# Optimization experiments

Hardware: AMD Instinct MI355X
Metric: run time of the kernel (lower is better)

## Reference

```python
import jax, jax.numpy as jnp
import numpy as np

B, T, I, H, O = 1024, 128, 128, 1024, 64


def setup_inputs() -> dict:
    key = jax.random.key(0)
    ks = jax.random.split(key, 7)
    s_i = 1.0 / np.sqrt(H)
    return {
        "x": jax.random.normal(ks[0], (B, T * I), dtype=jnp.float32),
        "w_ih": jax.random.uniform(ks[1], (4 * H, I), minval=-s_i, maxval=s_i, dtype=jnp.float32),
        "w_hh": jax.random.uniform(ks[2], (4 * H, H), minval=-s_i, maxval=s_i, dtype=jnp.float32),
        "b_ih": jax.random.uniform(ks[3], (4 * H,), minval=-s_i, maxval=s_i, dtype=jnp.float32),
        "b_hh": jax.random.uniform(ks[4], (4 * H,), minval=-s_i, maxval=s_i, dtype=jnp.float32),
        "w_fc": jax.random.uniform(ks[5], (O, H), minval=-s_i, maxval=s_i, dtype=jnp.float32),
        "b_fc": jax.random.uniform(ks[6], (O,), minval=-s_i, maxval=s_i, dtype=jnp.float32),
    }


def reference(x, w_ih, w_hh, b_ih, b_hh, w_fc, b_fc):
    b = x.shape[0]
    i_dim = w_ih.shape[1]
    h_dim = w_hh.shape[1]
    t = x.shape[1] // i_dim
    # chunk(dim=1) into t contiguous slices == reshape [b, t, i]
    xs = x.reshape(b, t, i_dim)
    # precompute input-to-gate projection for all timesteps in one GEMM
    xg = jnp.einsum("bti,gi->tbg", xs, w_ih) + (b_ih + b_hh)  # [t, b, 4h]

    def step(carry, xg_t):
        h, c = carry
        gates = xg_t + h @ w_hh.T  # [b, 4h]
        ig, fg, gg, og = jnp.split(gates, 4, axis=-1)  # PyTorch LSTMCell gate order
        c_new = jax.nn.sigmoid(fg) * c + jax.nn.sigmoid(ig) * jnp.tanh(gg)
        h_new = jax.nn.sigmoid(og) * jnp.tanh(c_new)
        return (h_new, c_new), None

    h0 = jnp.zeros((b, h_dim), dtype=x.dtype)
    c0 = jnp.zeros((b, h_dim), dtype=x.dtype)
    (h_t, _), _ = jax.lax.scan(step, (h0, c0), xg)
    return h_t @ w_fc.T + b_fc
```

## Files before the change

### kernel.cpp

```cpp
#include <hip/hip_runtime.h>


#define B_DIM 1024
#define H_DIM 1024
#define I_DIM 128
#define T_DIM 128
#define XROW  (T_DIM * I_DIM)
#define KDIM  (I_DIM + H_DIM)
#define GDIM  (4 * H_DIM)
#define O_DIM 64

typedef float f32x4 __attribute__((ext_vector_type(4)));
typedef short bf16x8 __attribute__((ext_vector_type(8)));
typedef unsigned short u16x8 __attribute__((ext_vector_type(8)));

__device__ __forceinline__ unsigned short f2bf(float f) {
    union { float f; unsigned int u; } v; v.f = f;
    unsigned int r = v.u + 0x7fffu + ((v.u >> 16) & 1u);
    return (unsigned short)(r >> 16);
}
__device__ __forceinline__ float bf2f(unsigned short b) {
    union { unsigned int u; float f; } v; v.u = ((unsigned int)b) << 16;
    return v.f;
}
__device__ __forceinline__ float sigm(float x) { return 1.f / (1.f + __expf(-x)); }
__device__ __forceinline__ float tanh_fast(float x) { return 2.f / (1.f + __expf(-2.f * x)) - 1.f; }

__global__ void conv_x(const float* __restrict__ x, unsigned short* __restrict__ xb) {
    size_t i = ((size_t)blockIdx.x * 256 + threadIdx.x) * 8;
    float4 v0 = *(const float4*)(x + i);
    float4 v1 = *(const float4*)(x + i + 4);
    u16x8 o;
    o[0] = f2bf(v0.x); o[1] = f2bf(v0.y); o[2] = f2bf(v0.z); o[3] = f2bf(v0.w);
    o[4] = f2bf(v1.x); o[5] = f2bf(v1.y); o[6] = f2bf(v1.z); o[7] = f2bf(v1.w);
    *(u16x8*)(xb + i) = o;
}

__global__ void build_w(const float* __restrict__ w_ih, const float* __restrict__ w_hh,
                        const float* __restrict__ b_ih, const float* __restrict__ b_hh,
                        unsigned short* __restrict__ W, float* __restrict__ bias) {
    int r = blockIdx.x;
    int nb = r >> 7, q = r & 127;
    int wh = q >> 6, w = q & 63;
    int gate = w >> 4, jl = w & 15;
    int orig = gate * 1024 + nb * 32 + wh * 16 + jl;
    for (int k = threadIdx.x; k < KDIM; k += 256) {
        float v = (k < I_DIM) ? w_ih[(size_t)orig * I_DIM + k]
                              : w_hh[(size_t)orig * H_DIM + (k - I_DIM)];
        W[(size_t)r * KDIM + k] = f2bf(v);
    }
    if (threadIdx.x == 0) bias[r] = b_ih[orig] + b_hh[orig];
}

__global__ void trans_wfc(const float* __restrict__ w_fc, float* __restrict__ wT) {
    int o = blockIdx.x;
    for (int k = threadIdx.x; k < H_DIM; k += 256)
        wT[(size_t)k * O_DIM + o] = w_fc[(size_t)o * H_DIM + k];
}

__global__ void zero_hc(unsigned short* __restrict__ h0, float* __restrict__ c) {
    int idx = blockIdx.x * 256 + threadIdx.x;
    h0[idx] = 0;
    c[idx] = 0.f;
}

#define READ_TILE(OFF) do {                                                       \
    asm volatile("ds_read_b128 %0, %1 offset:" OFF : "=v"(fa0) : "v"(aA0));       \
    asm volatile("ds_read_b128 %0, %1 offset:" OFF : "=v"(fa1) : "v"(aA1));       \
    asm volatile("ds_read_b128 %0, %1 offset:" OFF : "=v"(fb0) : "v"(aB0));       \
    asm volatile("ds_read_b128 %0, %1 offset:" OFF : "=v"(fb1) : "v"(aB1));       \
    asm volatile("ds_read_b128 %0, %1 offset:" OFF : "=v"(fb2) : "v"(aB2));       \
    asm volatile("ds_read_b128 %0, %1 offset:" OFF : "=v"(fb3) : "v"(aB3));       \
    asm volatile("ds_read_b128 %0, %1 offset:" OFF : "=v"(ga0) : "v"(aA0x));      \
    asm volatile("ds_read_b128 %0, %1 offset:" OFF : "=v"(ga1) : "v"(aA1x));      \
    asm volatile("ds_read_b128 %0, %1 offset:" OFF : "=v"(gb0) : "v"(aB0x));      \
    asm volatile("ds_read_b128 %0, %1 offset:" OFF : "=v"(gb1) : "v"(aB1x));      \
    asm volatile("ds_read_b128 %0, %1 offset:" OFF : "=v"(gb2) : "v"(aB2x));      \
    asm volatile("ds_read_b128 %0, %1 offset:" OFF : "=v"(gb3) : "v"(aB3x));      \
    asm volatile("s_waitcnt lgkmcnt(0)" ::: "memory");                            \
    __builtin_amdgcn_sched_barrier(0);                                            \
} while (0)

#define MFMA_(a, b, c) c = __builtin_amdgcn_mfma_f32_16x16x32_bf16(a, b, c, 0, 0, 0)
#define MM_TILE() do {                                                            \
    MFMA_(fa0, fb0, acc[0][0]); MFMA_(fa0, fb1, acc[0][1]);                       \
    MFMA_(fa0, fb2, acc[0][2]); MFMA_(fa0, fb3, acc[0][3]);                       \
    MFMA_(fa1, fb0, acc[1][0]); MFMA_(fa1, fb1, acc[1][1]);                       \
    MFMA_(fa1, fb2, acc[1][2]); MFMA_(fa1, fb3, acc[1][3]);                       \
    MFMA_(ga0, gb0, acc[0][0]); MFMA_(ga0, gb1, acc[0][1]);                       \
    MFMA_(ga0, gb2, acc[0][2]); MFMA_(ga0, gb3, acc[0][3]);                       \
    MFMA_(ga1, gb0, acc[1][0]); MFMA_(ga1, gb1, acc[1][1]);                       \
    MFMA_(ga1, gb2, acc[1][2]); MFMA_(ga1, gb3, acc[1][3]);                       \
} while (0)

__global__ __launch_bounds__(512, 2)
void lstm_step(const unsigned short* __restrict__ xb,
               const unsigned short* __restrict__ W,
               const float* __restrict__ bias,
               const unsigned short* __restrict__ h_in,
               unsigned short* __restrict__ h_out,
               float* __restrict__ c_st,
               int t) {
    __shared__ __align__(16) unsigned short lds[4 * 8192];
    const int tid  = threadIdx.x;
    const int wv   = tid >> 6, lane = tid & 63;
    const int wm   = wv >> 1, wn = wv & 1;
    const int quad = lane >> 4, l16 = lane & 15;
    const int l7   = l16 & 7;
    const int bid = blockIdx.x;
    const int xcd = bid & 7;
    const int sl  = bid >> 3;
    const int nb  = xcd * 4 + (sl & 3);
    const int mb  = sl >> 2;

    const int j  = nb * 32 + wn * 16 + l16;
    const int bb = nb * 128 + wn * 64 + l16;
    const float bi  = bias[bb +  0];
    const float bf_ = bias[bb + 16];
    const float bg  = bias[bb + 32];
    const float bo  = bias[bb + 48];
    float cold[2][4];
#pragma unroll
    for (int mi = 0; mi < 2; mi++)
#pragma unroll
        for (int r = 0; r < 4; r++) {
            const int brow = mb * 128 + wm * 32 + mi * 16 + quad * 4 + r;
            cold[mi][r] = c_st[(size_t)brow * H_DIM + j];
        }

    f32x4 acc[2][4];
#pragma unroll
    for (int i = 0; i < 2; i++)
#pragma unroll
        for (int jj = 0; jj < 4; jj++) acc[i][jj] = f32x4{0.f, 0.f, 0.f, 0.f};

    const int arow = lane >> 3;
    const int ag   = lane & 7;
    const int colperm = ((ag ^ arow) << 3);

    auto stage = [&](int bsel, int ks) {
        const int kt = ks * 64;
        unsigned short* As_ = lds + bsel * 16384;
        unsigned short* Bs_ = As_ + 8192;
#pragma unroll
        for (int c4 = 0; c4 < 2; ++c4) {
            const int row0 = wv * 16 + c4 * 8;
            const int row  = row0 + arow;
            const unsigned short* srcA =
                (kt < I_DIM)
                    ? xb   + (size_t)(mb * 128 + row) * XROW + t * I_DIM + kt + colperm
                    : h_in + (size_t)(mb * 128 + row) * H_DIM + (kt - I_DIM) + colperm;
            __builtin_amdgcn_global_load_lds(
                (const __attribute__((address_space(1))) void*)srcA,
                (__attribute__((address_space(3))) void*)(&As_[row0 * 64]), 16, 0, 0);
        }
#pragma unroll
        for (int c4 = 0; c4 < 2; ++c4) {
            const int row0 = wv * 16 + c4 * 8;
            const int row  = row0 + arow;
            const unsigned short* srcB =
                W + (size_t)(nb * 128 + row) * KDIM + kt + colperm;
            __builtin_amdgcn_global_load_lds(
                (const __attribute__((address_space(1))) void*)srcB,
                (__attribute__((address_space(3))) void*)(&Bs_[row0 * 64]), 16, 0, 0);
        }
    };

    const unsigned lbase = (unsigned)(unsigned long long)
        (__attribute__((address_space(3))) void*)lds;
    const unsigned cp  = (unsigned)((quad ^ l7) << 4);
    const unsigned aA0 = lbase + (unsigned)((wm * 32 + l16) * 128) + cp;
    const unsigned aA1 = aA0 + 2048;
    const unsigned aB0 = lbase + 16384u + (unsigned)((wn * 64 + l16) * 128) + cp;
    const unsigned aB1 = aB0 + 2048;
    const unsigned aB2 = aB0 + 4096;
    const unsigned aB3 = aB0 + 6144;
    const unsigned aA0x = aA0 ^ 64u, aA1x = aA1 ^ 64u;
    const unsigned aB0x = aB0 ^ 64u, aB1x = aB1 ^ 64u;
    const unsigned aB2x = aB2 ^ 64u, aB3x = aB3 ^ 64u;
    bf16x8 fa0, fa1, fb0, fb1, fb2, fb3, ga0, ga1, gb0, gb1, gb2, gb3;

    stage(0, 0);
    stage(1, 1);
#pragma unroll 1
    for (int p = 0; p < 8; ++p) {
        asm volatile("s_waitcnt vmcnt(4)" ::: "memory");
        __builtin_amdgcn_s_barrier();
        READ_TILE("0");
        __builtin_amdgcn_s_barrier();
        stage(0, 2 * p + 2);
        MM_TILE();

        asm volatile("s_waitcnt vmcnt(4)" ::: "memory");
        __builtin_amdgcn_s_barrier();
        READ_TILE("32768");
        __builtin_amdgcn_s_barrier();
        stage(1, 2 * p + 3);
        MM_TILE();
    }
    asm volatile("s_waitcnt vmcnt(4)" ::: "memory");
    __builtin_amdgcn_s_barrier();
    READ_TILE("0");
    MM_TILE();
    asm volatile("s_waitcnt vmcnt(0)" ::: "memory");
    __builtin_amdgcn_s_barrier();
    READ_TILE("32768");
    MM_TILE();

#pragma unroll
    for (int mi = 0; mi < 2; mi++) {
#pragma unroll
        for (int r = 0; r < 4; r++) {
            const int brow = mb * 128 + wm * 32 + mi * 16 + quad * 4 + r;
            const float gi = acc[mi][0][r] + bi;
            const float gf = acc[mi][1][r] + bf_;
            const float gg = acc[mi][2][r] + bg;
            const float go = acc[mi][3][r] + bo;
            const size_t idx = (size_t)brow * H_DIM + j;
            const float cn = sigm(gf) * cold[mi][r] + sigm(gi) * tanh_fast(gg);
            c_st[idx] = cn;
            h_out[idx] = f2bf(sigm(go) * tanh_fast(cn));
        }
    }
}

__global__ void proj(const unsigned short* __restrict__ h,
                     const float* __restrict__ wT,
                     const float* __restrict__ b_fc,
                     float* __restrict__ out) {
    __shared__ float hs[4][H_DIM];
    const int tid = threadIdx.x, wv = tid >> 6, o = tid & 63;
    const int b = blockIdx.x * 4 + wv;
    const unsigned short* hrow = h + (size_t)b * H_DIM;
#pragma unroll
    for (int i = 0; i < 2; ++i) {
        const int k0 = i * 512 + o * 8;
        u16x8 v = *(const u16x8*)(hrow + k0);
        float4 f0 = {bf2f((unsigned short)v[0]), bf2f((unsigned short)v[1]),
                     bf2f((unsigned short)v[2]), bf2f((unsigned short)v[3])};
        float4 f1 = {bf2f((unsigned short)v[4]), bf2f((unsigned short)v[5]),
                     bf2f((unsigned short)v[6]), bf2f((unsigned short)v[7])};
        *(float4*)&hs[wv][k0]     = f0;
        *(float4*)&hs[wv][k0 + 4] = f1;
    }
    float s0 = 0.f, s1 = 0.f, s2 = 0.f, s3 = 0.f;
#pragma unroll 4
    for (int k4 = 0; k4 < H_DIM / 4; ++k4) {
        float4 hv = *(const float4*)&hs[wv][k4 * 4];
        const float* wp = wT + (size_t)k4 * 4 * O_DIM + o;
        s0 += hv.x * wp[0 * O_DIM];
        s1 += hv.y * wp[1 * O_DIM];
        s2 += hv.z * wp[2 * O_DIM];
        s3 += hv.w * wp[3 * O_DIM];
    }
    out[(size_t)b * O_DIM + o] = s0 + s1 + s2 + s3 + b_fc[o];
}

extern "C" void kernel_launch(void* const* d_in, const int* in_sizes, int n_in,
                              void* d_out, int out_size, void* d_ws, size_t ws_size,
                              hipStream_t stream) {
    const float* x    = (const float*)d_in[0];
    const float* w_ih = (const float*)d_in[1];
    const float* w_hh = (const float*)d_in[2];
    const float* b_ih = (const float*)d_in[3];
    const float* b_hh = (const float*)d_in[4];
    const float* w_fc = (const float*)d_in[5];
    const float* b_fc = (const float*)d_in[6];
    float* out = (float*)d_out;

    char* ws = (char*)d_ws;
    size_t off = 0;
    unsigned short* xb = (unsigned short*)(ws + off); off += (size_t)B_DIM * XROW * 2;
    unsigned short* W  = (unsigned short*)(ws + off); off += (size_t)GDIM * KDIM * 2;
    float* bias        = (float*)(ws + off);          off += (size_t)GDIM * 4;
    unsigned short* h0 = (unsigned short*)(ws + off); off += (size_t)B_DIM * H_DIM * 2;
    unsigned short* h1 = (unsigned short*)(ws + off); off += (size_t)B_DIM * H_DIM * 2;
    float* c           = (float*)(ws + off);          off += (size_t)B_DIM * H_DIM * 4;
    float* wT          = (float*)(ws + off);          off += (size_t)H_DIM * O_DIM * 4;

    conv_x<<<8192, 256, 0, stream>>>(x, xb);
    build_w<<<GDIM, 256, 0, stream>>>(w_ih, w_hh, b_ih, b_hh, W, bias);
    trans_wfc<<<O_DIM, 256, 0, stream>>>(w_fc, wT);
    zero_hc<<<4096, 256, 0, stream>>>(h0, c);

    for (int t = 0; t < T_DIM; ++t) {
        const unsigned short* hin = (t & 1) ? h1 : h0;
        unsigned short* hout      = (t & 1) ? h0 : h1;
        lstm_step<<<256, 512, 0, stream>>>(xb, W, bias, hin, hout, c, t);
    }
    proj<<<256, 256, 0, stream>>>(h0, wT, b_fc, out);
}
```

Before: 1.976 ms.

## Load A operands directly to registers, keep only B in LDS

The A operand (x slice and hidden state) is no longer staged through LDS. It is loaded straight into registers with global_load_dwordx4 in MFMA fragment layout and double-buffered across k-steps, so only the weight tile goes through LDS, which halves the shared-memory footprint. The aim is to cut LDS traffic and ds_read work per tile and raise occupancy headroom. In exchange it adds VGPR pressure for the prefetched A registers, uses uncoalesced per-lane global loads, and relies on fragile hand-tuned vmcnt counts.

```diff
diff --git a/kernel.cpp b/kernel.cpp
--- a/kernel.cpp
+++ b/kernel.cpp
@@ -64,15 +64,11 @@
     c[idx] = 0.f;
 }
 
-#define READ_TILE(OFF) do {                                                       \
-    asm volatile("ds_read_b128 %0, %1 offset:" OFF : "=v"(fa0) : "v"(aA0));       \
-    asm volatile("ds_read_b128 %0, %1 offset:" OFF : "=v"(fa1) : "v"(aA1));       \
+#define READ_B(OFF) do {                                                          \
     asm volatile("ds_read_b128 %0, %1 offset:" OFF : "=v"(fb0) : "v"(aB0));       \
     asm volatile("ds_read_b128 %0, %1 offset:" OFF : "=v"(fb1) : "v"(aB1));       \
     asm volatile("ds_read_b128 %0, %1 offset:" OFF : "=v"(fb2) : "v"(aB2));       \
     asm volatile("ds_read_b128 %0, %1 offset:" OFF : "=v"(fb3) : "v"(aB3));       \
-    asm volatile("ds_read_b128 %0, %1 offset:" OFF : "=v"(ga0) : "v"(aA0x));      \
-    asm volatile("ds_read_b128 %0, %1 offset:" OFF : "=v"(ga1) : "v"(aA1x));      \
     asm volatile("ds_read_b128 %0, %1 offset:" OFF : "=v"(gb0) : "v"(aB0x));      \
     asm volatile("ds_read_b128 %0, %1 offset:" OFF : "=v"(gb1) : "v"(aB1x));      \
     asm volatile("ds_read_b128 %0, %1 offset:" OFF : "=v"(gb2) : "v"(aB2x));      \
@@ -81,16 +77,27 @@
     __builtin_amdgcn_sched_barrier(0);                                            \
 } while (0)
 
+#define ISSUE_A(T0, T1, T2, T3, V0, V1, BASE, O0, O1) do {                         \
+    asm volatile("global_load_dwordx4 %0, %1, %2 offset:" O0                       \
+                 : "=v"(T0) : "v"(V0), "s"(BASE));                                 \
+    asm volatile("global_load_dwordx4 %0, %1, %2 offset:" O0                       \
+                 : "=v"(T1) : "v"(V1), "s"(BASE));                                 \
+    asm volatile("global_load_dwordx4 %0, %1, %2 offset:" O1                       \
+                 : "=v"(T2) : "v"(V0), "s"(BASE));                                 \
+    asm volatile("global_load_dwordx4 %0, %1, %2 offset:" O1                       \
+                 : "=v"(T3) : "v"(V1), "s"(BASE));                                 \
+} while (0)
+
 #define MFMA_(a, b, c) c = __builtin_amdgcn_mfma_f32_16x16x32_bf16(a, b, c, 0, 0, 0)
-#define MM_TILE() do {                                                            \
-    MFMA_(fa0, fb0, acc[0][0]); MFMA_(fa0, fb1, acc[0][1]);                       \
-    MFMA_(fa0, fb2, acc[0][2]); MFMA_(fa0, fb3, acc[0][3]);                       \
-    MFMA_(fa1, fb0, acc[1][0]); MFMA_(fa1, fb1, acc[1][1]);                       \
-    MFMA_(fa1, fb2, acc[1][2]); MFMA_(fa1, fb3, acc[1][3]);                       \
-    MFMA_(ga0, gb0, acc[0][0]); MFMA_(ga0, gb1, acc[0][1]);                       \
-    MFMA_(ga0, gb2, acc[0][2]); MFMA_(ga0, gb3, acc[0][3]);                       \
-    MFMA_(ga1, gb0, acc[1][0]); MFMA_(ga1, gb1, acc[1][1]);                       \
-    MFMA_(ga1, gb2, acc[1][2]); MFMA_(ga1, gb3, acc[1][3]);                       \
+#define MM_TILE(A0, A1, A2, A3) do {                                              \
+    MFMA_(A0, fb0, acc[0][0]); MFMA_(A0, fb1, acc[0][1]);                         \
+    MFMA_(A0, fb2, acc[0][2]); MFMA_(A0, fb3, acc[0][3]);                         \
+    MFMA_(A1, fb0, acc[1][0]); MFMA_(A1, fb1, acc[1][1]);                         \
+    MFMA_(A1, fb2, acc[1][2]); MFMA_(A1, fb3, acc[1][3]);                         \
+    MFMA_(A2, gb0, acc[0][0]); MFMA_(A2, gb1, acc[0][1]);                         \
+    MFMA_(A2, gb2, acc[0][2]); MFMA_(A2, gb3, acc[0][3]);                         \
+    MFMA_(A3, gb0, acc[1][0]); MFMA_(A3, gb1, acc[1][1]);                         \
+    MFMA_(A3, gb2, acc[1][2]); MFMA_(A3, gb3, acc[1][3]);                         \
 } while (0)
 
 __global__ __launch_bounds__(512, 2)
@@ -101,7 +108,7 @@
                unsigned short* __restrict__ h_out,
                float* __restrict__ c_st,
                int t) {
-    __shared__ __align__(16) unsigned short lds[4 * 8192];
+    __shared__ __align__(16) unsigned short lds[2 * 8192];
     const int tid  = threadIdx.x;
     const int wv   = tid >> 6, lane = tid & 63;
     const int wm   = wv >> 1, wn = wv & 1;
@@ -138,22 +145,9 @@
     const int ag   = lane & 7;
     const int colperm = ((ag ^ arow) << 3);
 
-    auto stage = [&](int bsel, int ks) {
+    auto stageB = [&](int bsel, int ks) {
         const int kt = ks * 64;
-        unsigned short* As_ = lds + bsel * 16384;
-        unsigned short* Bs_ = As_ + 8192;
-#pragma unroll
-        for (int c4 = 0; c4 < 2; ++c4) {
-            const int row0 = wv * 16 + c4 * 8;
-            const int row  = row0 + arow;
-            const unsigned short* srcA =
-                (kt < I_DIM)
-                    ? xb   + (size_t)(mb * 128 + row) * XROW + t * I_DIM + kt + colperm
-                    : h_in + (size_t)(mb * 128 + row) * H_DIM + (kt - I_DIM) + colperm;
-            __builtin_amdgcn_global_load_lds(
-                (const __attribute__((address_space(1))) void*)srcA,
-                (__attribute__((address_space(3))) void*)(&As_[row0 * 64]), 16, 0, 0);
-        }
+        unsigned short* Bs_ = lds + bsel * 8192;
 #pragma unroll
         for (int c4 = 0; c4 < 2; ++c4) {
             const int row0 = wv * 16 + c4 * 8;
@@ -169,43 +163,59 @@
     const unsigned lbase = (unsigned)(unsigned long long)
         (__attribute__((address_space(3))) void*)lds;
     const unsigned cp  = (unsigned)((quad ^ l7) << 4);
-    const unsigned aA0 = lbase + (unsigned)((wm * 32 + l16) * 128) + cp;
-    const unsigned aA1 = aA0 + 2048;
-    const unsigned aB0 = lbase + 16384u + (unsigned)((wn * 64 + l16) * 128) + cp;
+    const unsigned aB0 = lbase + (unsigned)((wn * 64 + l16) * 128) + cp;
     const unsigned aB1 = aB0 + 2048;
     const unsigned aB2 = aB0 + 4096;
     const unsigned aB3 = aB0 + 6144;
-    const unsigned aA0x = aA0 ^ 64u, aA1x = aA1 ^ 64u;
     const unsigned aB0x = aB0 ^ 64u, aB1x = aB1 ^ 64u;
     const unsigned aB2x = aB2 ^ 64u, aB3x = aB3 ^ 64u;
-    bf16x8 fa0, fa1, fb0, fb1, fb2, fb3, ga0, ga1, gb0, gb1, gb2, gb3;
-
-    stage(0, 0);
-    stage(1, 1);
+    bf16x8 fb0, fb1, fb2, fb3, gb0, gb1, gb2, gb3;
+
+    const int rowA0 = mb * 128 + wm * 32 + l16;
+    const int rowA1 = rowA0 + 16;
+    unsigned voffX0 = (unsigned)((rowA0 * XROW + t * I_DIM + quad * 8) * 2);
+    unsigned voffX1 = (unsigned)((rowA1 * XROW + t * I_DIM + quad * 8) * 2);
+    unsigned voffH0 = (unsigned)((rowA0 * H_DIM + quad * 8) * 2);
+    unsigned voffH1 = (unsigned)((rowA1 * H_DIM + quad * 8) * 2);
+    bf16x8 pa0, pa1, pa2, pa3;
+    bf16x8 qa0, qa1, qa2, qa3;
+
+    stageB(0, 0);
+    ISSUE_A(pa0, pa1, pa2, pa3, voffX0, voffX1, xb, "0", "64");
+    ISSUE_A(qa0, qa1, qa2, qa3, voffX0, voffX1, xb, "128", "192");
+    stageB(1, 1);
+
+    asm volatile("s_waitcnt vmcnt(6)" ::: "memory");
+    __builtin_amdgcn_s_barrier();
+    READ_B("0");
+    __builtin_amdgcn_s_barrier();
+    stageB(0, 2);
+    MM_TILE(pa0, pa1, pa2, pa3);
+
 #pragma unroll 1
     for (int p = 0; p < 8; ++p) {
-        asm volatile("s_waitcnt vmcnt(4)" ::: "memory");
+        asm volatile("s_waitcnt vmcnt(2)" ::: "memory");
         __builtin_amdgcn_s_barrier();
-        READ_TILE("0");
+        READ_B("16384");
         __builtin_amdgcn_s_barrier();
-        stage(0, 2 * p + 2);
-        MM_TILE();
-
-        asm volatile("s_waitcnt vmcnt(4)" ::: "memory");
+        ISSUE_A(pa0, pa1, pa2, pa3, voffH0, voffH1, h_in, "0", "64");
+        voffH0 += 128; voffH1 += 128;
+        stageB(1, 2 * p + 3);
+        MM_TILE(qa0, qa1, qa2, qa3);
+
+        asm volatile("s_waitcnt vmcnt(2)" ::: "memory");
         __builtin_amdgcn_s_barrier();
-        READ_TILE("32768");
+        READ_B("0");
         __builtin_amdgcn_s_barrier();
-        stage(1, 2 * p + 3);
-        MM_TILE();
-    }
-    asm volatile("s_waitcnt vmcnt(4)" ::: "memory");
-    __builtin_amdgcn_s_barrier();
-    READ_TILE("0");
-    MM_TILE();
+        ISSUE_A(qa0, qa1, qa2, qa3, voffH0, voffH1, h_in, "0", "64");
+        voffH0 += 128; voffH1 += 128;
+        if (p < 7) stageB(0, 2 * p + 4);
+        MM_TILE(pa0, pa1, pa2, pa3);
+    }
     asm volatile("s_waitcnt vmcnt(0)" ::: "memory");
     __builtin_amdgcn_s_barrier();
-    READ_TILE("32768");
-    MM_TILE();
+    READ_B("16384");
+    MM_TILE(qa0, qa1, qa2, qa3);
 
 #pragma unroll
     for (int mi = 0; mi < 2; mi++) {
```

Result: slower. 3.948 ms (+99.8%).

## Halve threads per LSTM step block, give each wave a 64x64 tile

Applied to the files above, without the earlier changes.

Each block now runs 4 waves of 256 threads instead of 8. Each wave computes a 64x64 output tile with 16 accumulators instead of 32x64, which gives more register-level reuse of A and B fragments per LDS read. Staging issues 4 loads per operand per wave, and the prologue, main loop and epilogue are reorganised to match. The final tile splits its LDS wait so the first half of the MFMAs can start before all reads land. The cost is lower occupancy and fewer waves available to hide latency, plus higher register pressure.

```diff
diff --git a/kernel.cpp b/kernel.cpp
--- a/kernel.cpp
+++ b/kernel.cpp
@@ -67,33 +67,56 @@
 #define READ_TILE(OFF) do {                                                       \
     asm volatile("ds_read_b128 %0, %1 offset:" OFF : "=v"(fa0) : "v"(aA0));       \
     asm volatile("ds_read_b128 %0, %1 offset:" OFF : "=v"(fa1) : "v"(aA1));       \
+    asm volatile("ds_read_b128 %0, %1 offset:" OFF : "=v"(fa2) : "v"(aA2));       \
+    asm volatile("ds_read_b128 %0, %1 offset:" OFF : "=v"(fa3) : "v"(aA3));       \
     asm volatile("ds_read_b128 %0, %1 offset:" OFF : "=v"(fb0) : "v"(aB0));       \
     asm volatile("ds_read_b128 %0, %1 offset:" OFF : "=v"(fb1) : "v"(aB1));       \
     asm volatile("ds_read_b128 %0, %1 offset:" OFF : "=v"(fb2) : "v"(aB2));       \
     asm volatile("ds_read_b128 %0, %1 offset:" OFF : "=v"(fb3) : "v"(aB3));       \
-    asm volatile("ds_read_b128 %0, %1 offset:" OFF : "=v"(ga0) : "v"(aA0x));      \
-    asm volatile("ds_read_b128 %0, %1 offset:" OFF : "=v"(ga1) : "v"(aA1x));      \
-    asm volatile("ds_read_b128 %0, %1 offset:" OFF : "=v"(gb0) : "v"(aB0x));      \
-    asm volatile("ds_read_b128 %0, %1 offset:" OFF : "=v"(gb1) : "v"(aB1x));      \
-    asm volatile("ds_read_b128 %0, %1 offset:" OFF : "=v"(gb2) : "v"(aB2x));      \
-    asm volatile("ds_read_b128 %0, %1 offset:" OFF : "=v"(gb3) : "v"(aB3x));      \
-    asm volatile("s_waitcnt lgkmcnt(0)" ::: "memory");                            \
-    __builtin_amdgcn_sched_barrier(0);                                            \
+    asm volatile("ds_read_b128 %0, %1 offset:" OFF : "=v"(ga0) : "v"(aA0 ^ 64u)); \
+    asm volatile("ds_read_b128 %0, %1 offset:" OFF : "=v"(ga1) : "v"(aA1 ^ 64u)); \
+    asm volatile("ds_read_b128 %0, %1 offset:" OFF : "=v"(ga2) : "v"(aA2 ^ 64u)); \
+    asm volatile("ds_read_b128 %0, %1 offset:" OFF : "=v"(ga3) : "v"(aA3 ^ 64u)); \
+    asm volatile("ds_read_b128 %0, %1 offset:" OFF : "=v"(gb0) : "v"(aB0 ^ 64u)); \
+    asm volatile("ds_read_b128 %0, %1 offset:" OFF : "=v"(gb1) : "v"(aB1 ^ 64u)); \
+    asm volatile("ds_read_b128 %0, %1 offset:" OFF : "=v"(gb2) : "v"(aB2 ^ 64u)); \
+    asm volatile("ds_read_b128 %0, %1 offset:" OFF : "=v"(gb3) : "v"(aB3 ^ 64u)); \
 } while (0)
 
 #define MFMA_(a, b, c) c = __builtin_amdgcn_mfma_f32_16x16x32_bf16(a, b, c, 0, 0, 0)
-#define MM_TILE() do {                                                            \
+
+#define MM_HALF1() do {                                                           \
     MFMA_(fa0, fb0, acc[0][0]); MFMA_(fa0, fb1, acc[0][1]);                       \
     MFMA_(fa0, fb2, acc[0][2]); MFMA_(fa0, fb3, acc[0][3]);                       \
     MFMA_(fa1, fb0, acc[1][0]); MFMA_(fa1, fb1, acc[1][1]);                       \
     MFMA_(fa1, fb2, acc[1][2]); MFMA_(fa1, fb3, acc[1][3]);                       \
+    MFMA_(fa2, fb0, acc[2][0]); MFMA_(fa2, fb1, acc[2][1]);                       \
+    MFMA_(fa2, fb2, acc[2][2]); MFMA_(fa2, fb3, acc[2][3]);                       \
+    MFMA_(fa3, fb0, acc[3][0]); MFMA_(fa3, fb1, acc[3][1]);                       \
+    MFMA_(fa3, fb2, acc[3][2]); MFMA_(fa3, fb3, acc[3][3]);                       \
+} while (0)
+#define MM_HALF2() do {                                                           \
     MFMA_(ga0, gb0, acc[0][0]); MFMA_(ga0, gb1, acc[0][1]);                       \
     MFMA_(ga0, gb2, acc[0][2]); MFMA_(ga0, gb3, acc[0][3]);                       \
     MFMA_(ga1, gb0, acc[1][0]); MFMA_(ga1, gb1, acc[1][1]);                       \
     MFMA_(ga1, gb2, acc[1][2]); MFMA_(ga1, gb3, acc[1][3]);                       \
+    MFMA_(ga2, gb0, acc[2][0]); MFMA_(ga2, gb1, acc[2][1]);                       \
+    MFMA_(ga2, gb2, acc[2][2]); MFMA_(ga2, gb3, acc[2][3]);                       \
+    MFMA_(ga3, gb0, acc[3][0]); MFMA_(ga3, gb1, acc[3][1]);                       \
+    MFMA_(ga3, gb2, acc[3][2]); MFMA_(ga3, gb3, acc[3][3]);                       \
 } while (0)
 
-__global__ __launch_bounds__(512, 2)
+#define DO_TILE(OFF) do {                                                         \
+    READ_TILE(OFF);                                                               \
+    asm volatile("s_waitcnt lgkmcnt(8)" ::: "memory");                            \
+    __builtin_amdgcn_sched_barrier(0);                                            \
+    MM_HALF1();                                                                   \
+    asm volatile("s_waitcnt lgkmcnt(0)" ::: "memory");                            \
+    __builtin_amdgcn_sched_barrier(0);                                            \
+    MM_HALF2();                                                                   \
+} while (0)
+
+__global__ __launch_bounds__(256, 1)
 void lstm_step(const unsigned short* __restrict__ xb,
                const unsigned short* __restrict__ W,
                const float* __restrict__ bias,
@@ -101,7 +124,7 @@
                unsigned short* __restrict__ h_out,
                float* __restrict__ c_st,
                int t) {
-    __shared__ __align__(16) unsigned short lds[4 * 8192];
+    __shared__ __align__(16) unsigned short lds[2 * 16384];
     const int tid  = threadIdx.x;
     const int wv   = tid >> 6, lane = tid & 63;
     const int wm   = wv >> 1, wn = wv & 1;
@@ -119,18 +142,18 @@
     const float bf_ = bias[bb + 16];
     const float bg  = bias[bb + 32];
     const float bo  = bias[bb + 48];
-    float cold[2][4];
-#pragma unroll
-    for (int mi = 0; mi < 2; mi++)
+    float cold[4][4];
+#pragma unroll
+    for (int mi = 0; mi < 4; mi++)
 #pragma unroll
         for (int r = 0; r < 4; r++) {
-            const int brow = mb * 128 + wm * 32 + mi * 16 + quad * 4 + r;
+            const int brow = mb * 128 + wm * 64 + mi * 16 + quad * 4 + r;
             cold[mi][r] = c_st[(size_t)brow * H_DIM + j];
         }
 
-    f32x4 acc[2][4];
-#pragma unroll
-    for (int i = 0; i < 2; i++)
+    f32x4 acc[4][4];
+#pragma unroll
+    for (int i = 0; i < 4; i++)
 #pragma unroll
         for (int jj = 0; jj < 4; jj++) acc[i][jj] = f32x4{0.f, 0.f, 0.f, 0.f};
 
@@ -143,8 +166,8 @@
         unsigned short* As_ = lds + bsel * 16384;
         unsigned short* Bs_ = As_ + 8192;
 #pragma unroll
-        for (int c4 = 0; c4 < 2; ++c4) {
-            const int row0 = wv * 16 + c4 * 8;
+        for (int c4 = 0; c4 < 4; ++c4) {
+            const int row0 = wv * 32 + c4 * 8;
             const int row  = row0 + arow;
             const unsigned short* srcA =
                 (kt < I_DIM)
@@ -155,8 +178,8 @@
                 (__attribute__((address_space(3))) void*)(&As_[row0 * 64]), 16, 0, 0);
         }
 #pragma unroll
-        for (int c4 = 0; c4 < 2; ++c4) {
-            const int row0 = wv * 16 + c4 * 8;
+        for (int c4 = 0; c4 < 4; ++c4) {
+            const int row0 = wv * 32 + c4 * 8;
             const int row  = row0 + arow;
             const unsigned short* srcB =
                 W + (size_t)(nb * 128 + row) * KDIM + kt + colperm;
@@ -169,49 +192,60 @@
     const unsigned lbase = (unsigned)(unsigned long long)
         (__attribute__((address_space(3))) void*)lds;
     const unsigned cp  = (unsigned)((quad ^ l7) << 4);
-    const unsigned aA0 = lbase + (unsigned)((wm * 32 + l16) * 128) + cp;
+    const unsigned aA0 = lbase + (unsigned)((wm * 64 + l16) * 128) + cp;
     const unsigned aA1 = aA0 + 2048;
+    const unsigned aA2 = aA0 + 4096;
+    const unsigned aA3 = aA0 + 6144;
     const unsigned aB0 = lbase + 16384u + (unsigned)((wn * 64 + l16) * 128) + cp;
     const unsigned aB1 = aB0 + 2048;
     const unsigned aB2 = aB0 + 4096;
     const unsigned aB3 = aB0 + 6144;
-    const unsigned aA0x = aA0 ^ 64u, aA1x = aA1 ^ 64u;
-    const unsigned aB0x = aB0 ^ 64u, aB1x = aB1 ^ 64u;
-    const unsigned aB2x = aB2 ^ 64u, aB3x = aB3 ^ 64u;
-    bf16x8 fa0, fa1, fb0, fb1, fb2, fb3, ga0, ga1, gb0, gb1, gb2, gb3;
+    bf16x8 fa0, fa1, fa2, fa3, fb0, fb1, fb2, fb3;
+    bf16x8 ga0, ga1, ga2, ga3, gb0, gb1, gb2, gb3;
 
     stage(0, 0);
     stage(1, 1);
+    asm volatile("s_waitcnt vmcnt(8)" ::: "memory");
+    __builtin_amdgcn_s_barrier();
+    READ_TILE("0");
+    asm volatile("s_waitcnt lgkmcnt(0)" ::: "memory");
+    __builtin_amdgcn_sched_barrier(0);
+    __builtin_amdgcn_s_barrier();
+    stage(0, 2);
+    MM_HALF1();
+    MM_HALF2();
+
 #pragma unroll 1
     for (int p = 0; p < 8; ++p) {
-        asm volatile("s_waitcnt vmcnt(4)" ::: "memory");
+        asm volatile("s_waitcnt vmcnt(8)" ::: "memory");
+        __builtin_amdgcn_s_barrier();
+        READ_TILE("32768");
+        asm volatile("s_waitcnt lgkmcnt(0)" ::: "memory");
+        __builtin_amdgcn_sched_barrier(0);
+        __builtin_amdgcn_s_barrier();
+        stage(1, 2 * p + 3);
+        MM_HALF1();
+        MM_HALF2();
+
+        asm volatile("s_waitcnt vmcnt(8)" ::: "memory");
         __builtin_amdgcn_s_barrier();
         READ_TILE("0");
+        asm volatile("s_waitcnt lgkmcnt(0)" ::: "memory");
+        __builtin_amdgcn_sched_barrier(0);
         __builtin_amdgcn_s_barrier();
-        stage(0, 2 * p + 2);
-        MM_TILE();
-
-        asm volatile("s_waitcnt vmcnt(4)" ::: "memory");
-        __builtin_amdgcn_s_barrier();
-        READ_TILE("32768");
-        __builtin_amdgcn_s_barrier();
-        stage(1, 2 * p + 3);
-        MM_TILE();
-    }
-    asm volatile("s_waitcnt vmcnt(4)" ::: "memory");
-    __builtin_amdgcn_s_barrier();
-    READ_TILE("0");
-    MM_TILE();
+        if (p < 7) stage(0, 2 * p + 4);
+        MM_HALF1();
+        MM_HALF2();
+    }
     asm volatile("s_waitcnt vmcnt(0)" ::: "memory");
     __builtin_amdgcn_s_barrier();
-    READ_TILE("32768");
-    MM_TILE();
-
-#pragma unroll
-    for (int mi = 0; mi < 2; mi++) {
+    DO_TILE("32768");
+
+#pragma unroll
+    for (int mi = 0; mi < 4; mi++) {
 #pragma unroll
         for (int r = 0; r < 4; r++) {
-            const int brow = mb * 128 + wm * 32 + mi * 16 + quad * 4 + r;
+            const int brow = mb * 128 + wm * 64 + mi * 16 + quad * 4 + r;
             const float gi = acc[mi][0][r] + bi;
             const float gf = acc[mi][1][r] + bf_;
             const float gg = acc[mi][2][r] + bg;
@@ -286,7 +320,7 @@
     for (int t = 0; t < T_DIM; ++t) {
         const unsigned short* hin = (t & 1) ? h1 : h0;
         unsigned short* hout      = (t & 1) ? h0 : h1;
-        lstm_step<<<256, 512, 0, stream>>>(xb, W, bias, hin, hout, c, t);
+        lstm_step<<<256, 256, 0, stream>>>(xb, W, bias, hin, hout, c, t);
     }
     proj<<<256, 256, 0, stream>>>(h0, wT, b_fc, out);
 }
```

Measured after the change: 2.104 ms. 6.5% more time.

## Deepen LSTM step GEMM pipeline to a four-stage LDS ring buffer

Applied to the files above, without the earlier changes.

Shared memory grows from two to four staging slots. The K-loop now prefetches three tiles ahead, and the barrier between reading a tile and refilling that slot is removed, so each k-tile pays one barrier instead of two. The goal is to hide more global-to-LDS latency in each latency-bound timestep GEMM. In exchange, LDS use doubles to 128 KB per block, which can limit how many blocks fit on a CU, and the vmcnt bookkeeping is hand-tuned and fragile.

```diff
diff --git a/kernel.cpp b/kernel.cpp
--- a/kernel.cpp
+++ b/kernel.cpp
@@ -64,19 +64,19 @@
     c[idx] = 0.f;
 }
 
-#define READ_TILE(OFF) do {                                                       \
-    asm volatile("ds_read_b128 %0, %1 offset:" OFF : "=v"(fa0) : "v"(aA0));       \
-    asm volatile("ds_read_b128 %0, %1 offset:" OFF : "=v"(fa1) : "v"(aA1));       \
-    asm volatile("ds_read_b128 %0, %1 offset:" OFF : "=v"(fb0) : "v"(aB0));       \
-    asm volatile("ds_read_b128 %0, %1 offset:" OFF : "=v"(fb1) : "v"(aB1));       \
-    asm volatile("ds_read_b128 %0, %1 offset:" OFF : "=v"(fb2) : "v"(aB2));       \
-    asm volatile("ds_read_b128 %0, %1 offset:" OFF : "=v"(fb3) : "v"(aB3));       \
-    asm volatile("ds_read_b128 %0, %1 offset:" OFF : "=v"(ga0) : "v"(aA0x));      \
-    asm volatile("ds_read_b128 %0, %1 offset:" OFF : "=v"(ga1) : "v"(aA1x));      \
-    asm volatile("ds_read_b128 %0, %1 offset:" OFF : "=v"(gb0) : "v"(aB0x));      \
-    asm volatile("ds_read_b128 %0, %1 offset:" OFF : "=v"(gb1) : "v"(aB1x));      \
-    asm volatile("ds_read_b128 %0, %1 offset:" OFF : "=v"(gb2) : "v"(aB2x));      \
-    asm volatile("ds_read_b128 %0, %1 offset:" OFF : "=v"(gb3) : "v"(aB3x));      \
+#define READ_TILE(A0, A1, B0, B1, B2, B3, OFF) do {                               \
+    asm volatile("ds_read_b128 %0, %1 offset:" OFF : "=v"(fa0) : "v"(A0));        \
+    asm volatile("ds_read_b128 %0, %1 offset:" OFF : "=v"(fa1) : "v"(A1));        \
+    asm volatile("ds_read_b128 %0, %1 offset:" OFF : "=v"(fb0) : "v"(B0));        \
+    asm volatile("ds_read_b128 %0, %1 offset:" OFF : "=v"(fb1) : "v"(B1));        \
+    asm volatile("ds_read_b128 %0, %1 offset:" OFF : "=v"(fb2) : "v"(B2));        \
+    asm volatile("ds_read_b128 %0, %1 offset:" OFF : "=v"(fb3) : "v"(B3));        \
+    asm volatile("ds_read_b128 %0, %1 offset:" OFF : "=v"(ga0) : "v"((A0) ^ 64u));\
+    asm volatile("ds_read_b128 %0, %1 offset:" OFF : "=v"(ga1) : "v"((A1) ^ 64u));\
+    asm volatile("ds_read_b128 %0, %1 offset:" OFF : "=v"(gb0) : "v"((B0) ^ 64u));\
+    asm volatile("ds_read_b128 %0, %1 offset:" OFF : "=v"(gb1) : "v"((B1) ^ 64u));\
+    asm volatile("ds_read_b128 %0, %1 offset:" OFF : "=v"(gb2) : "v"((B2) ^ 64u));\
+    asm volatile("ds_read_b128 %0, %1 offset:" OFF : "=v"(gb3) : "v"((B3) ^ 64u));\
     asm volatile("s_waitcnt lgkmcnt(0)" ::: "memory");                            \
     __builtin_amdgcn_sched_barrier(0);                                            \
 } while (0)
@@ -93,6 +93,11 @@
     MFMA_(ga1, gb2, acc[1][2]); MFMA_(ga1, gb3, acc[1][3]);                       \
 } while (0)
 
+#define WAITV(N) do {                                                             \
+    asm volatile("s_waitcnt vmcnt(" N ")" ::: "memory");                          \
+    __builtin_amdgcn_s_barrier();                                                 \
+} while (0)
+
 __global__ __launch_bounds__(512, 2)
 void lstm_step(const unsigned short* __restrict__ xb,
                const unsigned short* __restrict__ W,
@@ -101,7 +106,7 @@
                unsigned short* __restrict__ h_out,
                float* __restrict__ c_st,
                int t) {
-    __shared__ __align__(16) unsigned short lds[4 * 8192];
+    __shared__ __align__(16) unsigned short lds[8 * 8192];
     const int tid  = threadIdx.x;
     const int wv   = tid >> 6, lane = tid & 63;
     const int wm   = wv >> 1, wn = wv & 1;
@@ -175,36 +180,37 @@
     const unsigned aB1 = aB0 + 2048;
     const unsigned aB2 = aB0 + 4096;
     const unsigned aB3 = aB0 + 6144;
-    const unsigned aA0x = aA0 ^ 64u, aA1x = aA1 ^ 64u;
-    const unsigned aB0x = aB0 ^ 64u, aB1x = aB1 ^ 64u;
-    const unsigned aB2x = aB2 ^ 64u, aB3x = aB3 ^ 64u;
+    const unsigned cA0 = aA0 + 65536u, cA1 = aA1 + 65536u;
+    const unsigned cB0 = aB0 + 65536u, cB1 = aB1 + 65536u;
+    const unsigned cB2 = aB2 + 65536u, cB3 = aB3 + 65536u;
     bf16x8 fa0, fa1, fb0, fb1, fb2, fb3, ga0, ga1, gb0, gb1, gb2, gb3;
 
     stage(0, 0);
     stage(1, 1);
+    stage(2, 2);
+
 #pragma unroll 1
-    for (int p = 0; p < 8; ++p) {
-        asm volatile("s_waitcnt vmcnt(4)" ::: "memory");
-        __builtin_amdgcn_s_barrier();
-        READ_TILE("0");
-        __builtin_amdgcn_s_barrier();
-        stage(0, 2 * p + 2);
-        MM_TILE();
-
-        asm volatile("s_waitcnt vmcnt(4)" ::: "memory");
-        __builtin_amdgcn_s_barrier();
-        READ_TILE("32768");
-        __builtin_amdgcn_s_barrier();
-        stage(1, 2 * p + 3);
-        MM_TILE();
-    }
-    asm volatile("s_waitcnt vmcnt(4)" ::: "memory");
-    __builtin_amdgcn_s_barrier();
-    READ_TILE("0");
+    for (int q = 0; q < 3; ++q) {
+        WAITV("8"); READ_TILE(aA0, aA1, aB0, aB1, aB2, aB3, "0");
+        stage(3, 4 * q + 3); MM_TILE();
+        WAITV("8"); READ_TILE(aA0, aA1, aB0, aB1, aB2, aB3, "32768");
+        stage(0, 4 * q + 4); MM_TILE();
+        WAITV("8"); READ_TILE(cA0, cA1, cB0, cB1, cB2, cB3, "0");
+        stage(1, 4 * q + 5); MM_TILE();
+        WAITV("8"); READ_TILE(cA0, cA1, cB0, cB1, cB2, cB3, "32768");
+        stage(2, 4 * q + 6); MM_TILE();
+    }
+    WAITV("8"); READ_TILE(aA0, aA1, aB0, aB1, aB2, aB3, "0");
+    stage(3, 15); MM_TILE();
+    WAITV("8"); READ_TILE(aA0, aA1, aB0, aB1, aB2, aB3, "32768");
+    stage(0, 16); MM_TILE();
+    WAITV("8"); READ_TILE(cA0, cA1, cB0, cB1, cB2, cB3, "0");
+    stage(1, 17); MM_TILE();
+    WAITV("8"); READ_TILE(cA0, cA1, cB0, cB1, cB2, cB3, "32768");
     MM_TILE();
-    asm volatile("s_waitcnt vmcnt(0)" ::: "memory");
-    __builtin_amdgcn_s_barrier();
-    READ_TILE("32768");
+    WAITV("4"); READ_TILE(aA0, aA1, aB0, aB1, aB2, aB3, "0");
+    MM_TILE();
+    WAITV("0"); READ_TILE(aA0, aA1, aB0, aB1, aB2, aB3, "32768");
     MM_TILE();
 
 #pragma unroll
```

Result: faster. 1.816 ms (-8.1%).
